# Kernel optimization log

Hardware: AMD Instinct MI355X
Metric: run time of the kernel (lower is better)

Reference implementation:

```python
import jax, jax.numpy as jnp
import numpy as np

B, D, H, C, T, F = 4096, 1024, 2048, 1000, 819200, 32


def setup_inputs() -> dict:
    key = jax.random.key(0)
    ks = jax.random.split(key, 12)
    feature_vector = jax.random.normal(ks[0], (B, D), dtype=jnp.float32)
    var_flat = jax.random.normal(ks[1], (T, F), dtype=jnp.float32)
    segment_ids = jnp.sort(jax.random.randint(ks[2], (T,), 0, B))
    target_vector = jax.random.randint(ks[3], (B,), 0, C)
    target_scalar = jax.random.normal(ks[4], (B,), dtype=jnp.float32)
    # learned params (torch Linear convention: W [out, in])
    Wv = jax.random.normal(ks[5], (D, F), dtype=jnp.float32) / np.sqrt(F)
    bv = jnp.zeros((D,), dtype=jnp.float32)
    W1 = jax.random.normal(ks[6], (H, D), dtype=jnp.float32) / np.sqrt(D)
    b1 = jnp.zeros((H,), dtype=jnp.float32)
    W2 = jax.random.normal(ks[7], (C, H), dtype=jnp.float32) / np.sqrt(H)
    b2 = jnp.zeros((C,), dtype=jnp.float32)
    Ws = jax.random.normal(ks[8], (1, H), dtype=jnp.float32) / np.sqrt(H)
    bs = jnp.zeros((1,), dtype=jnp.float32)
    return {
        "feature_vector": feature_vector, "var_flat": var_flat,
        "segment_ids": segment_ids, "target_vector": target_vector,
        "target_scalar": target_scalar, "Wv": Wv, "bv": bv,
        "W1": W1, "b1": b1, "W2": W2, "b2": b2, "Ws": Ws, "bs": bs,
    }


def reference(feature_vector, var_flat, segment_ids, target_vector, target_scalar,
              Wv, bv, W1, b1, W2, b2, Ws, bs):
    nb = feature_vector.shape[0]
    # ragged per-item mean via segment reduce (replaces python loop)
    sums = jax.ops.segment_sum(var_flat, segment_ids, num_segments=nb)      # [B, 32]
    counts = jax.ops.segment_sum(jnp.ones((var_flat.shape[0],), var_flat.dtype),
                                 segment_ids, num_segments=nb)
    means = sums / jnp.maximum(counts, 1.0)[:, None]
    var_processed = means @ Wv.T + bv                                        # [B, D]
    combined = feature_vector + var_processed
    hidden = jax.nn.relu(combined @ W1.T + b1)                               # [B, H]
    vector_output = hidden @ W2.T + b2                                       # [B, C]
    scalar_output = (hidden @ Ws.T + bs).squeeze(-1)                         # [B]
    logp = jax.nn.log_softmax(vector_output, axis=-1)
    loss_vector = -jnp.mean(jnp.take_along_axis(logp, target_vector[:, None], axis=1))
    loss_scalar = jnp.mean(jnp.square(scalar_output - target_scalar))
    total_loss = loss_vector + loss_scalar
    acc = jnp.mean((jnp.argmax(vector_output, axis=1) == target_vector).astype(jnp.float32))
    return total_loss, loss_vector, loss_scalar, acc
```

## Files before the change

kernel.cpp:

```cpp
#include <hip/hip_runtime.h>
#include <hip/hip_bf16.h>
#include <math.h>

#define B_  4096
#define D_  1024
#define H_  2048
#define C_  1000
#define T_  819200
#define F_  32
#define NPAD2 1024
#define NPART 1024

typedef __attribute__((ext_vector_type(8))) short short8;
typedef __attribute__((ext_vector_type(4))) float f32x4;

static const size_t WS_SUMS     = 0;
static const size_t WS_COUNTS   = WS_SUMS + (size_t)B_ * F_ * 4;
static const size_t WS_ZERO_SZ  = WS_COUNTS + (size_t)B_ * 4;
static const size_t WS_PV       = WS_ZERO_SZ;
static const size_t WS_PA       = WS_PV + NPART * 4;
static const size_t WS_PS       = WS_PA + NPART * 4;
static const size_t WS_B2P      = WS_PS + NPART * 4;
static const size_t WS_COMBINED = 1u << 20;
static const size_t WS_W1BF     = WS_COMBINED + (size_t)B_ * D_ * 2;
static const size_t WS_W2BF     = WS_W1BF + (size_t)H_ * D_ * 2;
static const size_t WS_HIDDEN   = WS_W2BF + (size_t)NPAD2 * H_ * 2;
static const size_t WS_LOGITS   = WS_HIDDEN + (size_t)B_ * H_ * 2;

#define RPT 32
__global__ __launch_bounds__(256) void seg_reduce_kernel(
    const float* __restrict__ var_flat, const int* __restrict__ seg_ids,
    float* __restrict__ sums, float* __restrict__ counts) {
  int gt  = blockIdx.x * 256 + threadIdx.x;
  int c4  = (gt & 7) * 4;
  long base = (long)(gt >> 3) * RPT;
  int cur = -1;
  float a0 = 0.f, a1 = 0.f, a2 = 0.f, a3 = 0.f, cnt = 0.f;
  for (int r = 0; r < RPT; ++r) {
    long row = base + r;
    int s = seg_ids[row];
    float4 v = *(const float4*)(var_flat + row * F_ + c4);
    if (s != cur) {
      if (cur >= 0) {
        float* dst = &sums[(size_t)cur * F_ + c4];
        atomicAdd(dst + 0, a0); atomicAdd(dst + 1, a1);
        atomicAdd(dst + 2, a2); atomicAdd(dst + 3, a3);
        if (c4 == 0) atomicAdd(&counts[cur], cnt);
      }
      cur = s; a0 = a1 = a2 = a3 = 0.f; cnt = 0.f;
    }
    a0 += v.x; a1 += v.y; a2 += v.z; a3 += v.w; cnt += 1.f;
  }
  if (cur >= 0) {
    float* dst = &sums[(size_t)cur * F_ + c4];
    atomicAdd(dst + 0, a0); atomicAdd(dst + 1, a1);
    atomicAdd(dst + 2, a2); atomicAdd(dst + 3, a3);
    if (c4 == 0) atomicAdd(&counts[cur], cnt);
  }
}

__global__ __launch_bounds__(256) void cvt_bf16_kernel(
    const float* __restrict__ src, __hip_bfloat16* __restrict__ dst, int n8) {
  int i = blockIdx.x * 256 + threadIdx.x;
  if (i >= n8) return;
  size_t off = (size_t)i * 8;
  float4 a = *(const float4*)(src + off);
  float4 b = *(const float4*)(src + off + 4);
  __hip_bfloat16 t[8];
  t[0] = __float2bfloat16(a.x); t[1] = __float2bfloat16(a.y);
  t[2] = __float2bfloat16(a.z); t[3] = __float2bfloat16(a.w);
  t[4] = __float2bfloat16(b.x); t[5] = __float2bfloat16(b.y);
  t[6] = __float2bfloat16(b.z); t[7] = __float2bfloat16(b.w);
  *(uint4*)(dst + off) = *(uint4*)t;
}

__global__ __launch_bounds__(256) void cvt_w2_kernel(
    const float* __restrict__ W2, const float* __restrict__ Ws,
    __hip_bfloat16* __restrict__ dst) {
  int i = blockIdx.x * 256 + threadIdx.x;
  size_t off = (size_t)i * 8;
  int row = (int)(off / H_);
  __hip_bfloat16 t[8];
  const float* src = nullptr;
  if (row < C_)       src = W2 + off;
  else if (row == C_) src = Ws + (off - (size_t)C_ * H_);
  if (src) {
    float4 a = *(const float4*)(src);
    float4 b = *(const float4*)(src + 4);
    t[0] = __float2bfloat16(a.x); t[1] = __float2bfloat16(a.y);
    t[2] = __float2bfloat16(a.z); t[3] = __float2bfloat16(a.w);
    t[4] = __float2bfloat16(b.x); t[5] = __float2bfloat16(b.y);
    t[6] = __float2bfloat16(b.z); t[7] = __float2bfloat16(b.w);
  } else {
    for (int e = 0; e < 8; ++e) t[e] = __float2bfloat16(0.f);
  }
  *(uint4*)(dst + off) = *(uint4*)t;
}

__global__ __launch_bounds__(256) void pad_bias_kernel(
    const float* __restrict__ b2, const float* __restrict__ bs,
    float* __restrict__ b2p) {
  int i = blockIdx.x * 256 + threadIdx.x;
  float v = 0.f;
  if (i < C_) v = b2[i];
  else if (i == C_) v = bs[0];
  b2p[i] = v;
}

__global__ __launch_bounds__(256) void combined_kernel(
    const float* __restrict__ feat, const float* __restrict__ sums,
    const float* __restrict__ counts, const float* __restrict__ Wv,
    const float* __restrict__ bv, __hip_bfloat16* __restrict__ combined) {
  __shared__ float m[8][F_];
  int b0  = blockIdx.y * 8;
  int tid = threadIdx.x;
  {
    int seg = tid >> 5, col = tid & 31;
    float c = counts[b0 + seg];
    c = c < 1.f ? 1.f : c;
    m[seg][col] = sums[(size_t)(b0 + seg) * F_ + col] / c;
  }
  __syncthreads();
  int d = blockIdx.x * 256 + tid;
  float w[F_];
  {
    const float4* wv = (const float4*)(Wv + (size_t)d * F_);
#pragma unroll
    for (int f4 = 0; f4 < F_ / 4; ++f4) {
      float4 x = wv[f4];
      w[f4 * 4 + 0] = x.x; w[f4 * 4 + 1] = x.y;
      w[f4 * 4 + 2] = x.z; w[f4 * 4 + 3] = x.w;
    }
  }
  float bvd = bv[d];
#pragma unroll
  for (int bb = 0; bb < 8; ++bb) {
    float acc = feat[(size_t)(b0 + bb) * D_ + d] + bvd;
#pragma unroll
    for (int f = 0; f < F_; ++f) acc = fmaf(m[bb][f], w[f], acc);
    combined[(size_t)(b0 + bb) * D_ + d] = __float2bfloat16(acc);
  }
}

__device__ inline void load16_lds(const short* g, short* l) {
  __builtin_amdgcn_global_load_lds(
      (const __attribute__((address_space(1))) void*)g,
      (__attribute__((address_space(3))) void*)l, 16, 0, 0);
}

template <int MODE>
__global__ __launch_bounds__(256) void gemm_mfma_kernel(
    const short* __restrict__ A, const short* __restrict__ Bm,
    const float* __restrict__ bias, void* __restrict__ Cout,
    int M, int K, int Nout) {
  __shared__ short As[2][4096];
  __shared__ short Bs[2][4096];
  const int tid  = threadIdx.x;
  const int lane = tid & 63;
  const int w    = tid >> 6;
  const int bm = blockIdx.y * 128;
  const int bn = blockIdx.x * 128;
  const int wm = (w >> 1) * 64;
  const int wn = (w & 1) * 64;
  const int m_lane = lane & 15;
  const int quad   = lane >> 4;

  f32x4 acc[4][4];
#pragma unroll
  for (int i = 0; i < 4; ++i)
#pragma unroll
    for (int j = 0; j < 4; ++j) acc[i][j] = f32x4{0.f, 0.f, 0.f, 0.f};

  const int c0 = w * 128 + lane;
  const int c1 = c0 + 64;
  const short* gA0 = A + (size_t)(bm + (c0 & 127)) * K + (c0 >> 7) * 8;
  const short* gA1 = A + (size_t)(bm + (c1 & 127)) * K + (c1 >> 7) * 8;
  const short* gB0 = Bm + (size_t)(bn + (c0 & 127)) * K + (c0 >> 7) * 8;
  const short* gB1 = Bm + (size_t)(bn + (c1 & 127)) * K + (c1 >> 7) * 8;
  const int l0 = w * 1024;
  const int l1 = l0 + 512;

  load16_lds(gA0, &As[0][l0]);
  load16_lds(gA1, &As[0][l1]);
  load16_lds(gB0, &Bs[0][l0]);
  load16_lds(gB1, &Bs[0][l1]);

  const int iters = K >> 5;
  for (int it = 0; it < iters; ++it) {
    const int cur = it & 1, nxt = cur ^ 1;
    __syncthreads();
    const int k1 = (it + 1) << 5;
    if (k1 < K) {
      load16_lds(gA0 + k1, &As[nxt][l0]);
      load16_lds(gA1 + k1, &As[nxt][l1]);
      load16_lds(gB0 + k1, &Bs[nxt][l0]);
      load16_lds(gB1 + k1, &Bs[nxt][l1]);
    }
    short8 af[4], bf[4];
#pragma unroll
    for (int i = 0; i < 4; ++i)
      af[i] = *(const short8*)&As[cur][quad * 1024 + (wm + i * 16 + m_lane) * 8];
#pragma unroll
    for (int j = 0; j < 4; ++j)
      bf[j] = *(const short8*)&Bs[cur][quad * 1024 + (wn + j * 16 + m_lane) * 8];
#pragma unroll
    for (int i = 0; i < 4; ++i)
#pragma unroll
      for (int j = 0; j < 4; ++j)
        acc[i][j] = __builtin_amdgcn_mfma_f32_16x16x32_bf16(af[i], bf[j], acc[i][j], 0, 0, 0);
  }

  const int row0 = bm + wm + quad * 4;
  const int col0 = bn + wn + m_lane;
  if (MODE == 0) {
    __hip_bfloat16* Cb = (__hip_bfloat16*)Cout;
#pragma unroll
    for (int j = 0; j < 4; ++j) {
      int col = col0 + j * 16;
      float bsv = bias[col];
#pragma unroll
      for (int i = 0; i < 4; ++i)
#pragma unroll
        for (int r = 0; r < 4; ++r) {
          int row = row0 + i * 16 + r;
          float v = acc[i][j][r] + bsv;
          v = v > 0.f ? v : 0.f;
          Cb[(size_t)row * Nout + col] = __float2bfloat16(v);
        }
    }
  } else {
    float* Cf = (float*)Cout;
#pragma unroll
    for (int j = 0; j < 4; ++j) {
      int col = col0 + j * 16;
      float bsv = bias[col];
#pragma unroll
      for (int i = 0; i < 4; ++i)
#pragma unroll
        for (int r = 0; r < 4; ++r) {
          int row = row0 + i * 16 + r;
          Cf[(size_t)row * Nout + col] = acc[i][j][r] + bsv;
        }
    }
  }
}

__global__ __launch_bounds__(256) void loss_kernel(
    const float* __restrict__ logits, const int* __restrict__ target,
    const float* __restrict__ tgt_scal,
    float* __restrict__ pv, float* __restrict__ pa, float* __restrict__ ps) {
  int tid  = threadIdx.x;
  int lane = tid & 63;
  int w    = tid >> 6;
  int b    = blockIdx.x * 4 + w;
  const float*  row  = logits + (size_t)b * NPAD2;
  const float4* row4 = (const float4*)row;
  float v[16];
  float vmax = -INFINITY;
  int   imax = 0x7fffffff;
#pragma unroll
  for (int k = 0; k < 4; ++k) {
    int c4 = lane + 64 * k;
    float4 x = row4[c4];
    float e0 = x.x, e1 = x.y, e2 = x.z, e3 = x.w;
    int idx = c4 * 4;
    if (idx + 0 >= C_) e0 = -INFINITY;
    if (idx + 1 >= C_) e1 = -INFINITY;
    if (idx + 2 >= C_) e2 = -INFINITY;
    if (idx + 3 >= C_) e3 = -INFINITY;
    v[k * 4 + 0] = e0; v[k * 4 + 1] = e1; v[k * 4 + 2] = e2; v[k * 4 + 3] = e3;
    if (e0 > vmax) { vmax = e0; imax = idx + 0; }
    if (e1 > vmax) { vmax = e1; imax = idx + 1; }
    if (e2 > vmax) { vmax = e2; imax = idx + 2; }
    if (e3 > vmax) { vmax = e3; imax = idx + 3; }
  }
#pragma unroll
  for (int o = 32; o > 0; o >>= 1) {
    float ov = __shfl_down(vmax, o, 64);
    int   oi = __shfl_down(imax, o, 64);
    if (ov > vmax || (ov == vmax && oi < imax)) { vmax = ov; imax = oi; }
  }
  vmax = __shfl(vmax, 0, 64);
  float se = 0.f;
#pragma unroll
  for (int j = 0; j < 16; ++j) se += expf(v[j] - vmax);
#pragma unroll
  for (int o = 32; o > 0; o >>= 1) se += __shfl_down(se, o, 64);
  __shared__ float s_nll[4], s_acc[4], s_sq[4];
  if (lane == 0) {
    int t = target[b];
    float logp = row[t] - vmax - logf(se);
    s_nll[w] = -logp;
    s_acc[w] = (imax == t) ? 1.f : 0.f;
    float d = row[C_] - tgt_scal[b];
    s_sq[w] = d * d;
  }
  __syncthreads();
  if (tid == 0) {
    pv[blockIdx.x] = s_nll[0] + s_nll[1] + s_nll[2] + s_nll[3];
    pa[blockIdx.x] = s_acc[0] + s_acc[1] + s_acc[2] + s_acc[3];
    ps[blockIdx.x] = s_sq[0] + s_sq[1] + s_sq[2] + s_sq[3];
  }
}

__global__ __launch_bounds__(256) void finalize_kernel(
    const float* __restrict__ pv, const float* __restrict__ pa,
    const float* __restrict__ ps, float* __restrict__ out) {
  int tid  = threadIdx.x;
  int lane = tid & 63;
  int w    = tid >> 6;
  float nll = 0.f, acc = 0.f, sq = 0.f;
  for (int i = tid; i < NPART; i += 256) {
    nll += pv[i]; acc += pa[i]; sq += ps[i];
  }
#pragma unroll
  for (int o = 32; o > 0; o >>= 1) {
    nll += __shfl_down(nll, o, 64);
    acc += __shfl_down(acc, o, 64);
    sq  += __shfl_down(sq,  o, 64);
  }
  __shared__ float sn[4], sa[4], ss[4];
  if (lane == 0) { sn[w] = nll; sa[w] = acc; ss[w] = sq; }
  __syncthreads();
  if (tid == 0) {
    float lv = (sn[0] + sn[1] + sn[2] + sn[3]) * (1.f / B_);
    float ls = (ss[0] + ss[1] + ss[2] + ss[3]) * (1.f / B_);
    float ac = (sa[0] + sa[1] + sa[2] + sa[3]) * (1.f / B_);
    out[0] = lv + ls;
    out[1] = lv;
    out[2] = ls;
    out[3] = ac;
  }
}

extern "C" void kernel_launch(void* const* d_in, const int* in_sizes, int n_in,
                              void* d_out, int out_size, void* d_ws, size_t ws_size,
                              hipStream_t stream) {
  const float* feature  = (const float*)d_in[0];
  const float* var_flat = (const float*)d_in[1];
  const int*   seg_ids  = (const int*)d_in[2];
  const int*   tgt_vec  = (const int*)d_in[3];
  const float* tgt_scal = (const float*)d_in[4];
  const float* Wv = (const float*)d_in[5];
  const float* bv = (const float*)d_in[6];
  const float* W1 = (const float*)d_in[7];
  const float* b1 = (const float*)d_in[8];
  const float* W2 = (const float*)d_in[9];
  const float* b2 = (const float*)d_in[10];
  const float* Ws = (const float*)d_in[11];
  const float* bs = (const float*)d_in[12];
  float* out = (float*)d_out;

  char* ws = (char*)d_ws;
  float* sums   = (float*)(ws + WS_SUMS);
  float* counts = (float*)(ws + WS_COUNTS);
  float* pv     = (float*)(ws + WS_PV);
  float* pa     = (float*)(ws + WS_PA);
  float* ps     = (float*)(ws + WS_PS);
  float* b2p    = (float*)(ws + WS_B2P);
  __hip_bfloat16* combined_bf = (__hip_bfloat16*)(ws + WS_COMBINED);
  __hip_bfloat16* W1bf        = (__hip_bfloat16*)(ws + WS_W1BF);
  __hip_bfloat16* W2bf        = (__hip_bfloat16*)(ws + WS_W2BF);
  __hip_bfloat16* hidden_bf   = (__hip_bfloat16*)(ws + WS_HIDDEN);
  float*          logits      = (float*)(ws + WS_LOGITS);

  hipMemsetAsync(ws, 0, WS_ZERO_SZ, stream);

  seg_reduce_kernel<<<(T_ / RPT) * 8 / 256, 256, 0, stream>>>(var_flat, seg_ids, sums, counts);

  cvt_bf16_kernel<<<(H_ * D_ / 8 + 255) / 256, 256, 0, stream>>>(W1, W1bf, H_ * D_ / 8);
  cvt_w2_kernel<<<(NPAD2 * H_ / 8) / 256, 256, 0, stream>>>(W2, Ws, W2bf);
  pad_bias_kernel<<<NPAD2 / 256, 256, 0, stream>>>(b2, bs, b2p);

  {
    dim3 grid(D_ / 256, B_ / 8);
    combined_kernel<<<grid, 256, 0, stream>>>(feature, sums, counts, Wv, bv, combined_bf);
  }

  {
    dim3 grid(H_ / 128, B_ / 128);
    gemm_mfma_kernel<0><<<grid, 256, 0, stream>>>(
        (const short*)combined_bf, (const short*)W1bf, b1, hidden_bf, B_, D_, H_);
  }

  {
    dim3 grid(NPAD2 / 128, B_ / 128);
    gemm_mfma_kernel<1><<<grid, 256, 0, stream>>>(
        (const short*)hidden_bf, (const short*)W2bf, b2p, logits, B_, H_, NPAD2);
  }

  loss_kernel<<<B_ / 4, 256, 0, stream>>>(logits, tgt_vec, tgt_scal, pv, pa, ps);

  finalize_kernel<<<1, 256, 0, stream>>>(pv, pa, ps, out);
}
```

Baseline: 336.1 us.

## Halve GEMM M-tile to 64 and batch segment-reduce row loads by 8

The MFMA GEMM block tile shrinks from 128x128 to 64x128, halving A staging in LDS and per-wave accumulators, which doubles the grid size for both GEMMs. This targets low CU occupancy and tail effects: the second GEMM had only 256 blocks on a 256-CU part. The segment reduction now loads 8 segment ids and 8 rows at once, with a fast path when all 8 rows share a segment, to raise memory-level parallelism. The smaller tile lowers data reuse per block and adds global/LDS traffic for B.

```diff
diff --git a/kernel.cpp b/kernel.cpp
--- a/kernel.cpp
+++ b/kernel.cpp
@@ -36,27 +36,39 @@
   long base = (long)(gt >> 3) * RPT;
   int cur = -1;
   float a0 = 0.f, a1 = 0.f, a2 = 0.f, a3 = 0.f, cnt = 0.f;
-  for (int r = 0; r < RPT; ++r) {
-    long row = base + r;
-    int s = seg_ids[row];
-    float4 v = *(const float4*)(var_flat + row * F_ + c4);
-    if (s != cur) {
-      if (cur >= 0) {
-        float* dst = &sums[(size_t)cur * F_ + c4];
-        atomicAdd(dst + 0, a0); atomicAdd(dst + 1, a1);
-        atomicAdd(dst + 2, a2); atomicAdd(dst + 3, a3);
-        if (c4 == 0) atomicAdd(&counts[cur], cnt);
+#define FLUSH_SEG()                                              \
+  if (cur >= 0) {                                                \
+    float* dst = &sums[(size_t)cur * F_ + c4];                   \
+    atomicAdd(dst + 0, a0); atomicAdd(dst + 1, a1);              \
+    atomicAdd(dst + 2, a2); atomicAdd(dst + 3, a3);              \
+    if (c4 == 0) atomicAdd(&counts[cur], cnt);                   \
+    a0 = a1 = a2 = a3 = 0.f; cnt = 0.f;                          \
+  }
+  for (int rr = 0; rr < RPT; rr += 8) {
+    int4 sa = *(const int4*)(seg_ids + base + rr);
+    int4 sb = *(const int4*)(seg_ids + base + rr + 4);
+    float4 v[8];
+#pragma unroll
+    for (int e = 0; e < 8; ++e)
+      v[e] = *(const float4*)(var_flat + (base + rr + e) * F_ + c4);
+    int s[8] = {sa.x, sa.y, sa.z, sa.w, sb.x, sb.y, sb.z, sb.w};
+    if (s[0] == s[7]) {
+      if (s[0] != cur) { FLUSH_SEG(); cur = s[0]; }
+#pragma unroll
+      for (int e = 0; e < 8; ++e) {
+        a0 += v[e].x; a1 += v[e].y; a2 += v[e].z; a3 += v[e].w;
       }
-      cur = s; a0 = a1 = a2 = a3 = 0.f; cnt = 0.f;
+      cnt += 8.f;
+    } else {
+#pragma unroll
+      for (int e = 0; e < 8; ++e) {
+        if (s[e] != cur) { FLUSH_SEG(); cur = s[e]; }
+        a0 += v[e].x; a1 += v[e].y; a2 += v[e].z; a3 += v[e].w; cnt += 1.f;
+      }
     }
-    a0 += v.x; a1 += v.y; a2 += v.z; a3 += v.w; cnt += 1.f;
-  }
-  if (cur >= 0) {
-    float* dst = &sums[(size_t)cur * F_ + c4];
-    atomicAdd(dst + 0, a0); atomicAdd(dst + 1, a1);
-    atomicAdd(dst + 2, a2); atomicAdd(dst + 3, a3);
-    if (c4 == 0) atomicAdd(&counts[cur], cnt);
-  }
+  }
+  FLUSH_SEG();
+#undef FLUSH_SEG
 }
 
 __global__ __launch_bounds__(256) void cvt_bf16_kernel(
@@ -153,37 +165,36 @@
     const short* __restrict__ A, const short* __restrict__ Bm,
     const float* __restrict__ bias, void* __restrict__ Cout,
     int M, int K, int Nout) {
-  __shared__ short As[2][4096];
+  __shared__ short As[2][2048];
   __shared__ short Bs[2][4096];
   const int tid  = threadIdx.x;
   const int lane = tid & 63;
   const int w    = tid >> 6;
-  const int bm = blockIdx.y * 128;
+  const int bm = blockIdx.y * 64;
   const int bn = blockIdx.x * 128;
-  const int wm = (w >> 1) * 64;
+  const int wm = (w >> 1) * 32;
   const int wn = (w & 1) * 64;
   const int m_lane = lane & 15;
   const int quad   = lane >> 4;
 
-  f32x4 acc[4][4];
-#pragma unroll
-  for (int i = 0; i < 4; ++i)
+  f32x4 acc[2][4];
+#pragma unroll
+  for (int i = 0; i < 2; ++i)
 #pragma unroll
     for (int j = 0; j < 4; ++j) acc[i][j] = f32x4{0.f, 0.f, 0.f, 0.f};
 
-  const int c0 = w * 128 + lane;
-  const int c1 = c0 + 64;
-  const short* gA0 = A + (size_t)(bm + (c0 & 127)) * K + (c0 >> 7) * 8;
-  const short* gA1 = A + (size_t)(bm + (c1 & 127)) * K + (c1 >> 7) * 8;
-  const short* gB0 = Bm + (size_t)(bn + (c0 & 127)) * K + (c0 >> 7) * 8;
-  const short* gB1 = Bm + (size_t)(bn + (c1 & 127)) * K + (c1 >> 7) * 8;
-  const int l0 = w * 1024;
-  const int l1 = l0 + 512;
-
-  load16_lds(gA0, &As[0][l0]);
-  load16_lds(gA1, &As[0][l1]);
-  load16_lds(gB0, &Bs[0][l0]);
-  load16_lds(gB1, &Bs[0][l1]);
+  const short* gA = A + (size_t)(bm + lane) * K + w * 8;
+  const int cb0 = w * 128 + lane;
+  const int cb1 = cb0 + 64;
+  const short* gB0 = Bm + (size_t)(bn + (cb0 & 127)) * K + w * 8;
+  const short* gB1 = Bm + (size_t)(bn + (cb1 & 127)) * K + w * 8;
+  const int lA = w * 512;
+  const int lB0 = w * 1024;
+  const int lB1 = lB0 + 512;
+
+  load16_lds(gA,  &As[0][lA]);
+  load16_lds(gB0, &Bs[0][lB0]);
+  load16_lds(gB1, &Bs[0][lB1]);
 
   const int iters = K >> 5;
   for (int it = 0; it < iters; ++it) {
@@ -191,20 +202,19 @@
     __syncthreads();
     const int k1 = (it + 1) << 5;
     if (k1 < K) {
-      load16_lds(gA0 + k1, &As[nxt][l0]);
-      load16_lds(gA1 + k1, &As[nxt][l1]);
-      load16_lds(gB0 + k1, &Bs[nxt][l0]);
-      load16_lds(gB1 + k1, &Bs[nxt][l1]);
+      load16_lds(gA + k1,  &As[nxt][lA]);
+      load16_lds(gB0 + k1, &Bs[nxt][lB0]);
+      load16_lds(gB1 + k1, &Bs[nxt][lB1]);
     }
-    short8 af[4], bf[4];
-#pragma unroll
-    for (int i = 0; i < 4; ++i)
-      af[i] = *(const short8*)&As[cur][quad * 1024 + (wm + i * 16 + m_lane) * 8];
+    short8 af[2], bf[4];
+#pragma unroll
+    for (int i = 0; i < 2; ++i)
+      af[i] = *(const short8*)&As[cur][quad * 512 + (wm + i * 16 + m_lane) * 8];
 #pragma unroll
     for (int j = 0; j < 4; ++j)
       bf[j] = *(const short8*)&Bs[cur][quad * 1024 + (wn + j * 16 + m_lane) * 8];
 #pragma unroll
-    for (int i = 0; i < 4; ++i)
+    for (int i = 0; i < 2; ++i)
 #pragma unroll
       for (int j = 0; j < 4; ++j)
         acc[i][j] = __builtin_amdgcn_mfma_f32_16x16x32_bf16(af[i], bf[j], acc[i][j], 0, 0, 0);
@@ -219,7 +229,7 @@
       int col = col0 + j * 16;
       float bsv = bias[col];
 #pragma unroll
-      for (int i = 0; i < 4; ++i)
+      for (int i = 0; i < 2; ++i)
 #pragma unroll
         for (int r = 0; r < 4; ++r) {
           int row = row0 + i * 16 + r;
@@ -235,7 +245,7 @@
       int col = col0 + j * 16;
       float bsv = bias[col];
 #pragma unroll
-      for (int i = 0; i < 4; ++i)
+      for (int i = 0; i < 2; ++i)
 #pragma unroll
         for (int r = 0; r < 4; ++r) {
           int row = row0 + i * 16 + r;
@@ -378,13 +388,13 @@
   }
 
   {
-    dim3 grid(H_ / 128, B_ / 128);
+    dim3 grid(H_ / 128, B_ / 64);
     gemm_mfma_kernel<0><<<grid, 256, 0, stream>>>(
         (const short*)combined_bf, (const short*)W1bf, b1, hidden_bf, B_, D_, H_);
   }
 
   {
-    dim3 grid(NPAD2 / 128, B_ / 128);
+    dim3 grid(NPAD2 / 128, B_ / 64);
     gemm_mfma_kernel<1><<<grid, 256, 0, stream>>>(
         (const short*)hidden_bf, (const short*)W2bf, b2p, logits, B_, H_, NPAD2);
   }
```

Measured after the change: 340.3 us. About the same (+1.2%).
